# Performance work log

Hardware: AMD Instinct MI355X
Metric: run time of the kernel (lower is better)

The kernel has to match this reference:

```python
import jax, jax.numpy as jnp
import numpy as np

N_QUBITS = 10
DIM = 2 ** N_QUBITS
W_MUL = (2.0 ** 0.5) * 5.0 ** (-0.5)  # he_std * lrmul, use_wscale=True, lrmul=1
MEASURE_QUBIT = 5


def _c(v):
    return v.astype(jnp.complex64)


def _m2(a, b, c, d):
    return jnp.stack([jnp.stack([a, b]), jnp.stack([c, d])])


_ZERO = jnp.zeros((), jnp.complex64)


def _rx(phi):
    c, s = _c(jnp.cos(phi / 2)), _c(jnp.sin(phi / 2))
    return _m2(c, -1j * s, -1j * s, c)


def _ry(phi):
    c, s = _c(jnp.cos(phi / 2)), _c(jnp.sin(phi / 2))
    return _m2(c, -s, s, c)


def _rz(phi):
    c, s = _c(jnp.cos(phi / 2)), _c(jnp.sin(phi / 2))
    return _m2(c - 1j * s, _ZERO, _ZERO, c + 1j * s)


_CNOT = jnp.array([[1, 0, 0, 0], [0, 1, 0, 0], [0, 0, 0, 1], [0, 0, 1, 0]], jnp.complex64)


def _expand(g, n, q):
    # kron(I_{2^q}, g, I_{2^{n-q-k}}) where g acts on qubits q..q+k-1
    k = int(np.log2(g.shape[0]))
    left = jnp.eye(2 ** q, dtype=jnp.complex64)
    right = jnp.eye(2 ** (n - q - k), dtype=jnp.complex64)
    return jnp.kron(left, jnp.kron(g, right))


def _layer_unitary(weight):
    w = weight * W_MUL
    U = jnp.eye(DIM, dtype=jnp.complex64)
    for sign in (1.0, -1.0):
        for q in range(N_QUBITS):
            U = _expand(_rx(sign * w[q]), N_QUBITS, q) @ U
            U = _expand(_ry(sign * w[q + 10]), N_QUBITS, q) @ U
            U = _expand(_rz(sign * w[q + 20]), N_QUBITS, q) @ U
        for q in range(1, N_QUBITS):
            U = _expand(_CNOT, N_QUBITS, q - 1) @ U
    return U


def _measure_affinity(rho, which_q):
    # Tr(rho @ Z_which_q) with Z_q = kron(I, Z, I); Z_q is diagonal
    z = jnp.array([1.0, -1.0], jnp.float32)
    zdiag = jnp.kron(jnp.ones(2 ** which_q, jnp.float32),
                     jnp.kron(z, jnp.ones(2 ** (N_QUBITS - which_q - 1), jnp.float32)))
    return jnp.sum(jnp.diagonal(rho).real * zdiag).astype(jnp.float32)


def setup_inputs() -> dict:
    key = jax.random.key(0)
    k1, k2 = jax.random.split(key)
    x = jax.random.normal(k1, (DIM, DIM), dtype=jnp.float32)
    weight = jax.random.uniform(k2, (30,), dtype=jnp.float32, minval=0.0, maxval=2.0 * np.pi)
    return {"x": x, "weight": weight}


def reference(x, weight):
    E = _layer_unitary(weight)
    rho = (E @ x.astype(jnp.complex64)) @ E.conj().T
    return _measure_affinity(rho, MEASURE_QUBIT)
```

## Files before the change

### kernel.cpp

```cpp
#include <hip/hip_runtime.h>

#define DIM 1024
#define NQ 10

__device__ __forceinline__ float2 cmul(float2 a, float2 b) {
    return make_float2(a.x * b.x - a.y * b.y, a.x * b.y + a.y * b.x);
}
__device__ __forceinline__ float2 cadd(float2 a, float2 b) {
    return make_float2(a.x + b.x, a.y + b.y);
}
__device__ __forceinline__ float2 csub(float2 a, float2 b) {
    return make_float2(a.x - b.x, a.y - b.y);
}
__device__ __forceinline__ float2 cconj(float2 a) { return make_float2(a.x, -a.y); }

__device__ __forceinline__ void mm2(const float2* A, const float2* B, float2* C) {
    C[0] = cadd(cmul(A[0], B[0]), cmul(A[1], B[2]));
    C[1] = cadd(cmul(A[0], B[1]), cmul(A[1], B[3]));
    C[2] = cadd(cmul(A[2], B[0]), cmul(A[3], B[2]));
    C[3] = cadd(cmul(A[2], B[1]), cmul(A[3], B[3]));
}

__device__ __forceinline__ void compute_gates(const float* __restrict__ weight,
                                              float2* G, float2* Msh, int tid) {
    if (tid < NQ) {
        int q = tid;
        const float WM = 0.632455532033676f;
        float px = weight[q]      * WM * 0.5f;
        float py = weight[q + 10] * WM * 0.5f;
        float pz = weight[q + 20] * WM * 0.5f;
        float cx = cosf(px), sx = sinf(px);
        float cy = cosf(py), sy = sinf(py);
        float cz = cosf(pz), sz = sinf(pz);
        {
            float2 Rx[4] = { {cx, 0.f}, {0.f, -sx}, {0.f, -sx}, {cx, 0.f} };
            float2 Ry[4] = { {cy, 0.f}, {-sy, 0.f}, {sy, 0.f}, {cy, 0.f} };
            float2 Rz[4] = { {cz, -sz}, {0.f, 0.f}, {0.f, 0.f}, {cz, sz} };
            float2 T[4], u[4];
            mm2(Ry, Rx, T);
            mm2(Rz, T, u);
            G[q * 4 + 0] = u[0]; G[q * 4 + 1] = u[1];
            G[q * 4 + 2] = u[2]; G[q * 4 + 3] = u[3];
        }
        if (Msh && q < 6) {
            float nsx = -sx, nsy = -sy, nsz = -sz;
            float2 Rx[4] = { {cx, 0.f}, {0.f, -nsx}, {0.f, -nsx}, {cx, 0.f} };
            float2 Ry[4] = { {cy, 0.f}, {-nsy, 0.f}, {nsy, 0.f}, {cy, 0.f} };
            float2 Rz[4] = { {cz, -nsz}, {0.f, 0.f}, {0.f, 0.f}, {cz, nsz} };
            float2 T[4], u2[4];
            mm2(Ry, Rx, T);
            mm2(Rz, T, u2);
            for (int i = 0; i < 2; i++)
                for (int j = 0; j < 2; j++) {
                    float2 v = csub(cmul(cconj(u2[0 * 2 + i]), u2[0 * 2 + j]),
                                    cmul(cconj(u2[1 * 2 + i]), u2[1 * 2 + j]));
                    Msh[q * 4 + i * 2 + j] = v;
                }
        }
    }
}

__global__ __launch_bounds__(256) void pass1(const float* __restrict__ x,
                                             const float* __restrict__ weight,
                                             float2* __restrict__ z,
                                             float* __restrict__ out) {
    __shared__ float2 G[40];
    int tid = threadIdx.x;
    compute_gates(weight, G, nullptr, tid);
    __syncthreads();
    if (blockIdx.x == 0 && tid == 0) out[0] = 0.f;

    int lane = tid & 63;
    int r = blockIdx.x * 4 + (tid >> 6);
    const float4* xp = (const float4*)(x + r * DIM + lane * 16);
    float2 v[16];
#pragma unroll
    for (int k = 0; k < 4; k++) {
        float4 a = xp[k];
        v[k * 4 + 0] = make_float2(a.x, 0.f);
        v[k * 4 + 1] = make_float2(a.y, 0.f);
        v[k * 4 + 2] = make_float2(a.z, 0.f);
        v[k * 4 + 3] = make_float2(a.w, 0.f);
    }
#pragma unroll
    for (int q = 0; q < 6; q++) {
        float2 u0 = cconj(G[q * 4]),     u1 = cconj(G[q * 4 + 1]);
        float2 u2 = cconj(G[q * 4 + 2]), u3 = cconj(G[q * 4 + 3]);
        const int X = 1 << (5 - q);
        bool up = (lane & X) != 0;
        float2 go = up ? u3 : u0;
        float2 gp = up ? u2 : u1;
#pragma unroll
        for (int j = 0; j < 16; j++) {
            float2 p;
            p.x = __shfl_xor(v[j].x, X, 64);
            p.y = __shfl_xor(v[j].y, X, 64);
            v[j] = cadd(cmul(go, v[j]), cmul(gp, p));
        }
    }
#pragma unroll
    for (int q = 6; q < 10; q++) {
        float2 u0 = cconj(G[q * 4]),     u1 = cconj(G[q * 4 + 1]);
        float2 u2 = cconj(G[q * 4 + 2]), u3 = cconj(G[q * 4 + 3]);
        const int h = 1 << (9 - q);
#pragma unroll
        for (int j0 = 0; j0 < 16; j0++) {
            if ((j0 & h) == 0) {
                int j1 = j0 | h;
                float2 s0 = v[j0], s1 = v[j1];
                v[j0] = cadd(cmul(u0, s0), cmul(u1, s1));
                v[j1] = cadd(cmul(u2, s0), cmul(u3, s1));
            }
        }
    }
    float4* zp = (float4*)(z + r * DIM + lane * 16);
#pragma unroll
    for (int k = 0; k < 8; k++)
        zp[k] = make_float4(v[2 * k].x, v[2 * k].y, v[2 * k + 1].x, v[2 * k + 1].y);
}

__device__ __forceinline__ float extract_col(int c, const float2 v[16], int lane,
                                             const float2* Msh) {
    int af = c;
    af ^= af >> 1; af ^= af >> 2; af ^= af >> 4; af ^= af >> 8;
    int t = af & 15;
    int a05 = af >> 4;
    float2 m6 = make_float2(1.f, 0.f);
#pragma unroll
    for (int q = 0; q < 6; q++) {
        int ia = (a05 >> (5 - q)) & 1;
        int ib = (lane >> (5 - q)) & 1;
        m6 = cmul(m6, Msh[q * 4 + ia * 2 + ib]);
    }
    int pl = lane;
    pl ^= pl >> 1; pl ^= pl >> 2; pl ^= pl >> 4;
    float acc = 0.f;
#pragma unroll
    for (int j = 0; j < 16; j++) {
        const int p4j = j ^ (j >> 1) ^ (j >> 2) ^ (j >> 3);
        const int parmask = (p4j & 1) ? 63 : 0;
        int bf = (p4j << 6) | (pl ^ parmask);
        int b05 = bf >> 4;
        float mx = __shfl(m6.x, b05, 64);
        float my = __shfl(m6.y, b05, 64);
        if ((bf & 15) == t) acc += mx * v[j].x - my * v[j].y;
    }
    return acc;
}

__global__ __launch_bounds__(128) void pass2(const float2* __restrict__ z,
                                             const float* __restrict__ weight,
                                             float* __restrict__ out) {
    __shared__ float2 G[40];
    __shared__ float2 Msh[24];
    int tid = threadIdx.x;
    compute_gates(weight, G, Msh, tid);
    __syncthreads();

    int lane = tid & 63;
    int c0 = blockIdx.x * 4 + (tid >> 6) * 2;
    float2 v0[16], v1[16];
#pragma unroll
    for (int j = 0; j < 16; j++) {
        float4 t = *(const float4*)(z + ((j << 6) + lane) * DIM + c0);
        v0[j] = make_float2(t.x, t.y);
        v1[j] = make_float2(t.z, t.w);
    }
#pragma unroll
    for (int q = 0; q < 4; q++) {
        float2 u0 = G[q * 4], u1 = G[q * 4 + 1], u2 = G[q * 4 + 2], u3 = G[q * 4 + 3];
        const int h = 8 >> q;
#pragma unroll
        for (int j0 = 0; j0 < 16; j0++) {
            if ((j0 & h) == 0) {
                int j1 = j0 | h;
                {
                    float2 s0 = v0[j0], s1 = v0[j1];
                    v0[j0] = cadd(cmul(u0, s0), cmul(u1, s1));
                    v0[j1] = cadd(cmul(u2, s0), cmul(u3, s1));
                }
                {
                    float2 s0 = v1[j0], s1 = v1[j1];
                    v1[j0] = cadd(cmul(u0, s0), cmul(u1, s1));
                    v1[j1] = cadd(cmul(u2, s0), cmul(u3, s1));
                }
            }
        }
    }
#pragma unroll
    for (int q = 4; q < 10; q++) {
        float2 u0 = G[q * 4], u1 = G[q * 4 + 1], u2 = G[q * 4 + 2], u3 = G[q * 4 + 3];
        const int X = 1 << (9 - q);
        bool up = (lane & X) != 0;
        float2 go = up ? u3 : u0;
        float2 gp = up ? u2 : u1;
#pragma unroll
        for (int j = 0; j < 16; j++) {
            float2 p0, p1;
            p0.x = __shfl_xor(v0[j].x, X, 64);
            p0.y = __shfl_xor(v0[j].y, X, 64);
            p1.x = __shfl_xor(v1[j].x, X, 64);
            p1.y = __shfl_xor(v1[j].y, X, 64);
            v0[j] = cadd(cmul(go, v0[j]), cmul(gp, p0));
            v1[j] = cadd(cmul(go, v1[j]), cmul(gp, p1));
        }
    }

    float acc = extract_col(c0, v0, lane, Msh) + extract_col(c0 + 1, v1, lane, Msh);
#pragma unroll
    for (int off = 32; off > 0; off >>= 1) acc += __shfl_xor(acc, off, 64);
    if (lane == 0) atomicAdd(out, acc);
}

extern "C" void kernel_launch(void* const* d_in, const int* in_sizes, int n_in,
                              void* d_out, int out_size, void* d_ws, size_t ws_size,
                              hipStream_t stream) {
    const float* x = (const float*)d_in[0];
    const float* weight = (const float*)d_in[1];
    float* out = (float*)d_out;

    float2* z = (float2*)d_ws + 8192;

    pass1<<<256, 256, 0, stream>>>(x, weight, z, out);
    pass2<<<256, 128, 0, stream>>>(z, weight, out);
}
```

Before: 86.43 us.

## Split pass2 column work across two waves with LDS exchange for first qubit

Pass2 now uses 256 threads per block, with each pair of wavefronts sharing a column pair: each wave holds half of the 16 row-chunks. The first qubit gate, which pairs the two halves, is applied by exchanging values through shared memory. Both halves then run the remaining gates and extraction independently. Per-wave partial sums are combined in shared memory before a single atomic per block. The aim is to halve register pressure and double the wave count, improving occupancy and latency hiding, at the cost of an LDS round trip and an extra barrier.

```diff
diff --git a/kernel.cpp b/kernel.cpp
--- a/kernel.cpp
+++ b/kernel.cpp
@@ -119,8 +119,8 @@
         zp[k] = make_float4(v[2 * k].x, v[2 * k].y, v[2 * k + 1].x, v[2 * k + 1].y);
 }
 
-__device__ __forceinline__ float extract_col(int c, const float2 v[16], int lane,
-                                             const float2* Msh) {
+__device__ __forceinline__ float extract_half(int c, const float2 v[8], int half,
+                                              int lane, const float2* Msh) {
     int af = c;
     af ^= af >> 1; af ^= af >> 2; af ^= af >> 4; af ^= af >> 8;
     int t = af & 15;
@@ -136,42 +136,68 @@
     pl ^= pl >> 1; pl ^= pl >> 2; pl ^= pl >> 4;
     float acc = 0.f;
 #pragma unroll
-    for (int j = 0; j < 16; j++) {
-        const int p4j = j ^ (j >> 1) ^ (j >> 2) ^ (j >> 3);
-        const int parmask = (p4j & 1) ? 63 : 0;
+    for (int jj = 0; jj < 8; jj++) {
+        int j = half * 8 + jj;
+        int p4j = j ^ (j >> 1) ^ (j >> 2) ^ (j >> 3);
+        int parmask = (p4j & 1) ? 63 : 0;
         int bf = (p4j << 6) | (pl ^ parmask);
         int b05 = bf >> 4;
         float mx = __shfl(m6.x, b05, 64);
         float my = __shfl(m6.y, b05, 64);
-        if ((bf & 15) == t) acc += mx * v[j].x - my * v[j].y;
+        if ((bf & 15) == t) acc += mx * v[jj].x - my * v[jj].y;
     }
     return acc;
 }
 
-__global__ __launch_bounds__(128) void pass2(const float2* __restrict__ z,
+__global__ __launch_bounds__(256) void pass2(const float2* __restrict__ z,
                                              const float* __restrict__ weight,
                                              float* __restrict__ out) {
     __shared__ float2 G[40];
     __shared__ float2 Msh[24];
+    __shared__ float2 ex[2 * 2 * 8 * 2 * 64];
+    __shared__ float part[4];
     int tid = threadIdx.x;
+    int lane = tid & 63;
+    int w = tid >> 6;
+    int pair = w >> 1;
+    int half = w & 1;
+    int c0 = blockIdx.x * 4 + pair * 2;
+
+    float2 v0[8], v1[8];
+#pragma unroll
+    for (int jj = 0; jj < 8; jj++) {
+        int j = half * 8 + jj;
+        float4 t = *(const float4*)(z + ((j << 6) + lane) * DIM + c0);
+        v0[jj] = make_float2(t.x, t.y);
+        v1[jj] = make_float2(t.z, t.w);
+    }
     compute_gates(weight, G, Msh, tid);
+    int sec = pair * 2 + half;
+#pragma unroll
+    for (int jj = 0; jj < 8; jj++) {
+        ex[((sec * 8 + jj) * 2 + 0) * 64 + lane] = v0[jj];
+        ex[((sec * 8 + jj) * 2 + 1) * 64 + lane] = v1[jj];
+    }
     __syncthreads();
-
-    int lane = tid & 63;
-    int c0 = blockIdx.x * 4 + (tid >> 6) * 2;
-    float2 v0[16], v1[16];
-#pragma unroll
-    for (int j = 0; j < 16; j++) {
-        float4 t = *(const float4*)(z + ((j << 6) + lane) * DIM + c0);
-        v0[j] = make_float2(t.x, t.y);
-        v1[j] = make_float2(t.z, t.w);
-    }
-#pragma unroll
-    for (int q = 0; q < 4; q++) {
+    {
+        float2 u0 = G[0], u1 = G[1], u2 = G[2], u3 = G[3];
+        float2 go = half ? u3 : u0;
+        float2 gp = half ? u2 : u1;
+        int other = pair * 2 + (1 - half);
+#pragma unroll
+        for (int jj = 0; jj < 8; jj++) {
+            float2 p0 = ex[((other * 8 + jj) * 2 + 0) * 64 + lane];
+            float2 p1 = ex[((other * 8 + jj) * 2 + 1) * 64 + lane];
+            v0[jj] = cadd(cmul(go, v0[jj]), cmul(gp, p0));
+            v1[jj] = cadd(cmul(go, v1[jj]), cmul(gp, p1));
+        }
+    }
+#pragma unroll
+    for (int q = 1; q < 4; q++) {
         float2 u0 = G[q * 4], u1 = G[q * 4 + 1], u2 = G[q * 4 + 2], u3 = G[q * 4 + 3];
         const int h = 8 >> q;
 #pragma unroll
-        for (int j0 = 0; j0 < 16; j0++) {
+        for (int j0 = 0; j0 < 8; j0++) {
             if ((j0 & h) == 0) {
                 int j1 = j0 | h;
                 {
@@ -195,21 +221,24 @@
         float2 go = up ? u3 : u0;
         float2 gp = up ? u2 : u1;
 #pragma unroll
-        for (int j = 0; j < 16; j++) {
+        for (int jj = 0; jj < 8; jj++) {
             float2 p0, p1;
-            p0.x = __shfl_xor(v0[j].x, X, 64);
-            p0.y = __shfl_xor(v0[j].y, X, 64);
-            p1.x = __shfl_xor(v1[j].x, X, 64);
-            p1.y = __shfl_xor(v1[j].y, X, 64);
-            v0[j] = cadd(cmul(go, v0[j]), cmul(gp, p0));
-            v1[j] = cadd(cmul(go, v1[j]), cmul(gp, p1));
-        }
-    }
-
-    float acc = extract_col(c0, v0, lane, Msh) + extract_col(c0 + 1, v1, lane, Msh);
+            p0.x = __shfl_xor(v0[jj].x, X, 64);
+            p0.y = __shfl_xor(v0[jj].y, X, 64);
+            p1.x = __shfl_xor(v1[jj].x, X, 64);
+            p1.y = __shfl_xor(v1[jj].y, X, 64);
+            v0[jj] = cadd(cmul(go, v0[jj]), cmul(gp, p0));
+            v1[jj] = cadd(cmul(go, v1[jj]), cmul(gp, p1));
+        }
+    }
+
+    float acc = extract_half(c0, v0, half, lane, Msh) +
+                extract_half(c0 + 1, v1, half, lane, Msh);
 #pragma unroll
     for (int off = 32; off > 0; off >>= 1) acc += __shfl_xor(acc, off, 64);
-    if (lane == 0) atomicAdd(out, acc);
+    if (lane == 0) part[w] = acc;
+    __syncthreads();
+    if (tid == 0) atomicAdd(out, part[0] + part[1] + part[2] + part[3]);
 }
 
 extern "C" void kernel_launch(void* const* d_in, const int* in_sizes, int n_in,
@@ -222,5 +251,5 @@
     float2* z = (float2*)d_ws + 8192;
 
     pass1<<<256, 256, 0, stream>>>(x, weight, z, out);
-    pass2<<<256, 128, 0, stream>>>(z, weight, out);
-}
+    pass2<<<256, 256, 0, stream>>>(z, weight, out);
+}
```

After: 81.19 us. 1.06x faster.
